# Performance work log

Hardware: AMD Instinct MI355X
Metric: run time of the kernel (lower is better)

Reference implementation:

```python
import jax, jax.numpy as jnp
import numpy as np

N = 50000
E = 600000
IN_C = 128
HID = 128
OUT_C = 2


def setup_inputs() -> dict:
    key = jax.random.key(0)
    ks = jax.random.split(key, 16)
    x = jax.random.normal(ks[0], (N, IN_C), dtype=jnp.float32)
    edge_index = jax.random.randint(ks[1], (2, E), 0, N, dtype=jnp.int64)
    s = 0.05
    # policy_net: Linear(2*in, 64) -> ReLU -> Linear(64, 1) -> Sigmoid
    W_p1 = jax.random.normal(ks[2], (64, 2 * IN_C), dtype=jnp.float32) * s
    b_p1 = jnp.zeros((64,), dtype=jnp.float32)
    W_p2 = jax.random.normal(ks[3], (1, 64), dtype=jnp.float32) * s
    b_p2 = jnp.zeros((1,), dtype=jnp.float32)
    # GCNConv weights (lin without bias + separate bias, PyG convention)
    W1 = jax.random.normal(ks[4], (HID, IN_C), dtype=jnp.float32) * s
    b1 = jnp.zeros((HID,), dtype=jnp.float32)
    W2 = jax.random.normal(ks[5], (HID, HID), dtype=jnp.float32) * s
    b2 = jnp.zeros((HID,), dtype=jnp.float32)
    W_lin = jax.random.normal(ks[6], (OUT_C, HID), dtype=jnp.float32) * s
    b_lin = jnp.zeros((OUT_C,), dtype=jnp.float32)
    return {"x": x, "edge_index": edge_index, "W_p1": W_p1, "b_p1": b_p1,
            "W_p2": W_p2, "b_p2": b_p2, "W1": W1, "b1": b1, "W2": W2,
            "b2": b2, "W_lin": W_lin, "b_lin": b_lin}


def gcn_conv(x, src, dst, edge_weight, W, b, n_nodes):
    # PyG GCNConv with normalize=True, add_self_loops=True, given edge_weight.
    loop = jnp.arange(n_nodes, dtype=src.dtype)
    s = jnp.concatenate([src, loop])
    d = jnp.concatenate([dst, loop])
    w = jnp.concatenate([edge_weight, jnp.ones((n_nodes,), x.dtype)])
    deg = jax.ops.segment_sum(w, d, num_segments=n_nodes)
    dinv = jnp.where(deg > 0, jax.lax.rsqrt(jnp.where(deg > 0, deg, 1.0)), 0.0)
    norm = dinv[s] * w * dinv[d]  # [E+N]
    xl = x @ W.T  # [N, out]
    msg = norm[:, None] * xl[s]  # gather + scale
    agg = jax.ops.segment_sum(msg, d, num_segments=n_nodes)
    return agg + b


def reference(x, edge_index, W_p1, b_p1, W_p2, b_p2, W1, b1, W2, b2, W_lin, b_lin):
    src, dst = edge_index[0], edge_index[1]
    # edge-weight policy MLP on gathered, concatenated endpoint features
    cat_feat = jnp.concatenate([x[src], x[dst]], axis=1)  # [E, 2*in]
    h = jax.nn.relu(cat_feat @ W_p1.T + b_p1)
    edge_weight = jax.nn.sigmoid(h @ W_p2.T + b_p2)[:, 0]  # [E]
    x1 = jax.nn.relu(gcn_conv(x, src, dst, edge_weight, W1, b1, N))
    x2 = jax.nn.relu(gcn_conv(x1, src, dst, edge_weight, W2, b2, N))
    out = x2 @ W_lin.T + b_lin
    return jax.nn.sigmoid(out)
```

## Files before the change

kernel.cpp:

```cpp
#include <hip/hip_runtime.h>
#include <hip/hip_bf16.h>

#define NN 50000
#define NE 600000
#define CPAD 16

typedef __attribute__((ext_vector_type(8))) short short8;
typedef __attribute__((ext_vector_type(8))) _Float16 half8;
typedef __attribute__((ext_vector_type(4))) float floatx4;

__device__ __forceinline__ short bf16_bits(float v) {
    __hip_bfloat16 h = __float2bfloat16(v);
    return *reinterpret_cast<short*>(&h);
}

__global__ void k_init_cvt(const int* __restrict__ raw, int* __restrict__ count,
                           int* __restrict__ flag, const float* __restrict__ wp1,
                           const float* __restrict__ w1, const float* __restrict__ w2,
                           __hip_bfloat16* __restrict__ wcatb, __hip_bfloat16* __restrict__ w1b,
                           __hip_bfloat16* __restrict__ w2b) {
    int i = blockIdx.x * blockDim.x + threadIdx.x;
    if (i < NN) {
        count[(size_t)i * CPAD] = 0;
    }
    if (i < 16384) {
        int r = i >> 7, c = i & 127;
        float v = (r < 64) ? wp1[r * 256 + c] : wp1[(r - 64) * 256 + 128 + c];
        wcatb[i] = __float2bfloat16(v);
    } else if (i < 32768) {
        w1b[i - 16384] = __float2bfloat16(w1[i - 16384]);
    } else if (i < 49152) {
        w2b[i - 32768] = __float2bfloat16(w2[i - 32768]);
    }
    if (blockIdx.x == 0) {
        if (threadIdx.x == 0) *flag = 0;
        __syncthreads();
        int any = 0;
        for (int j = threadIdx.x; j < 1024; j += 256) any |= raw[2 * j + 1];
        if (any) atomicOr(flag, 1);
    }
}

#define GG 782
__global__ __launch_bounds__(256) void k_uv(
    const float* __restrict__ x, const __hip_bfloat16* __restrict__ Wb,
    const float* __restrict__ bp1, _Float16* __restrict__ uvh,
    __hip_bfloat16* __restrict__ xb) {
    const int lane = threadIdx.x & 63;
    const int wave = threadIdx.x >> 6;
    const int col = lane & 15;
    const int quad = lane >> 4;

    short8 bfrag[4][8];
    const short* wp = (const short*)Wb;
#pragma unroll
    for (int tt = 0; tt < 8; ++tt) {
        int row = tt * 16 + col;
#pragma unroll
        for (int kk = 0; kk < 4; ++kk)
            bfrag[kk][tt] = *(const short8*)(wp + row * 128 + kk * 32 + quad * 8);
    }
    int tile = blockIdx.x * 4 + wave;
    if (tile >= NN / 16) return;
    int base = tile * 16;

    floatx4 acc[8];
#pragma unroll
    for (int t = 0; t < 8; ++t) acc[t] = (floatx4){0.f, 0.f, 0.f, 0.f};
#pragma unroll
    for (int kk = 0; kk < 4; ++kk) {
        const float* xrow = x + (size_t)(base + col) * 128 + kk * 32 + quad * 8;
        float4 f0 = ((const float4*)xrow)[0];
        float4 f1 = ((const float4*)xrow)[1];
        short8 afrag;
        afrag[0] = bf16_bits(f0.x); afrag[1] = bf16_bits(f0.y);
        afrag[2] = bf16_bits(f0.z); afrag[3] = bf16_bits(f0.w);
        afrag[4] = bf16_bits(f1.x); afrag[5] = bf16_bits(f1.y);
        afrag[6] = bf16_bits(f1.z); afrag[7] = bf16_bits(f1.w);
        *(short8*)((short*)xb + (size_t)(base + col) * 128 + kk * 32 + quad * 8) = afrag;
#pragma unroll
        for (int tt = 0; tt < 8; ++tt)
            acc[tt] = __builtin_amdgcn_mfma_f32_16x16x32_bf16(afrag, bfrag[kk][tt], acc[tt], 0, 0, 0);
    }
#pragma unroll
    for (int tt = 0; tt < 8; ++tt) {
        int n = tt * 16 + col;
        float badd = (tt >= 4) ? bp1[n - 64] : 0.f;
#pragma unroll
        for (int r = 0; r < 4; ++r) {
            int row = base + quad * 4 + r;
            uvh[(size_t)row * 128 + n] = (_Float16)(acc[tt][r] + badd);
        }
    }
}

#define GCNT 256
#define GPOL 9375
__global__ __launch_bounds__(256) void k_cnt_policy(
    const int* __restrict__ raw, const int* __restrict__ flag,
    int* __restrict__ count, int* __restrict__ rank,
    const _Float16* __restrict__ uvh, const float* __restrict__ wp2,
    const float* __restrict__ bp2, float* __restrict__ ew_flat) {
    const bool f32 = (*flag) != 0;
    const long long* r64 = (const long long*)raw;
    if (blockIdx.x < GCNT) {
        int tid = blockIdx.x * 256 + threadIdx.x;
        for (int e = tid; e < NE; e += GCNT * 256) {
            int d = f32 ? raw[NE + e] : (int)r64[NE + e];
            rank[e] = atomicAdd(&count[(size_t)d * CPAD], 1);
        }
        return;
    }
    int pb = blockIdx.x - GCNT;
    int wave = threadIdx.x >> 6, lane = threadIdx.x & 63;
    int g = lane >> 3, c = lane & 7;
    int e1 = pb * 64 + wave * 16 + g;
    int e2 = e1 + 8;
    int s1, d1, s2, d2;
    if (f32) {
        s1 = raw[e1]; d1 = raw[NE + e1];
        s2 = raw[e2]; d2 = raw[NE + e2];
    } else {
        s1 = (int)r64[e1]; d1 = (int)r64[NE + e1];
        s2 = (int)r64[e2]; d2 = (int)r64[NE + e2];
    }
    half8 u1 = *(const half8*)(uvh + (size_t)s1 * 128 + c * 8);
    half8 v1 = *(const half8*)(uvh + (size_t)d1 * 128 + 64 + c * 8);
    half8 u2 = *(const half8*)(uvh + (size_t)s2 * 128 + c * 8);
    half8 v2 = *(const half8*)(uvh + (size_t)d2 * 128 + 64 + c * 8);
    float w2v[8];
    const float4* w2p = (const float4*)(wp2 + c * 8);
    float4 wa = w2p[0], wb = w2p[1];
    w2v[0] = wa.x; w2v[1] = wa.y; w2v[2] = wa.z; w2v[3] = wa.w;
    w2v[4] = wb.x; w2v[5] = wb.y; w2v[6] = wb.z; w2v[7] = wb.w;
    float b2 = bp2[0];
    float p1 = 0.f, p2 = 0.f;
#pragma unroll
    for (int j = 0; j < 8; ++j) {
        float h1 = (float)u1[j] + (float)v1[j];
        float h2 = (float)u2[j] + (float)v2[j];
        h1 = h1 > 0.f ? h1 : 0.f;
        h2 = h2 > 0.f ? h2 : 0.f;
        p1 += h1 * w2v[j];
        p2 += h2 * w2v[j];
    }
    p1 += __shfl_xor(p1, 1, 64); p2 += __shfl_xor(p2, 1, 64);
    p1 += __shfl_xor(p1, 2, 64); p2 += __shfl_xor(p2, 2, 64);
    p1 += __shfl_xor(p1, 4, 64); p2 += __shfl_xor(p2, 4, 64);
    if (c == 0) {
        ew_flat[e1] = 1.f / (1.f + __expf(-(p1 + b2)));
        ew_flat[e2] = 1.f / (1.f + __expf(-(p2 + b2)));
    }
}

__global__ void k_scan_block(const int* __restrict__ count, int* __restrict__ tmp,
                             int* __restrict__ bsums) {
    __shared__ int s[512];
    int tid = threadIdx.x;
    int i = blockIdx.x * 512 + tid;
    s[tid] = (i < NN) ? count[(size_t)i * CPAD] : 0;
    __syncthreads();
    for (int off = 1; off < 512; off <<= 1) {
        int t = (tid >= off) ? s[tid - off] : 0;
        __syncthreads();
        s[tid] += t;
        __syncthreads();
    }
    if (i < NN) tmp[i] = s[tid];
    if (tid == 511) bsums[blockIdx.x] = s[511];
}

__global__ void k_finalize(const int* __restrict__ tmp, const int* __restrict__ bsums,
                           int* __restrict__ rowptr) {
    __shared__ int sb[128];
    int tid = threadIdx.x;
    if (tid < 128) sb[tid] = (tid < 98) ? bsums[tid] : 0;
    __syncthreads();
    for (int off = 1; off < 128; off <<= 1) {
        int t = (tid < 128 && tid >= off) ? sb[tid - off] : 0;
        __syncthreads();
        if (tid < 128) sb[tid] += t;
        __syncthreads();
    }
    int i = blockIdx.x * blockDim.x + tid;
    if (i >= NN) return;
    int blk = i >> 9;
    int add = blk ? sb[blk - 1] : 0;
    int incl = tmp[i] + add;
    rowptr[i + 1] = incl;
    if (i == 0) rowptr[0] = 0;
}

__global__ void k_fill(const int* __restrict__ raw, const int* __restrict__ flag,
                       const int* __restrict__ rank, const int* __restrict__ rowptr,
                       const float* __restrict__ ew_flat, int2* __restrict__ meta) {
    int e = blockIdx.x * blockDim.x + threadIdx.x;
    if (e >= NE) return;
    int s, d;
    if (*flag) {
        s = raw[e];
        d = raw[NE + e];
    } else {
        const long long* r64 = (const long long*)raw;
        s = (int)r64[e];
        d = (int)r64[NE + e];
    }
    int pos = rowptr[d] + rank[e];
    meta[pos] = make_int2(s, __float_as_int(ew_flat[e]));
}

__global__ __launch_bounds__(256) void k_deg(const int* __restrict__ rowptr,
                                             const int2* __restrict__ meta,
                                             float* __restrict__ deg) {
    int wid = (blockIdx.x * blockDim.x + threadIdx.x) >> 6;
    int lane = threadIdx.x & 63;
    if (wid >= NN) return;
    int beg = rowptr[wid], end = rowptr[wid + 1];
    float s = 0.f;
    for (int p = beg + lane; p < end; p += 64) s += __int_as_float(meta[p].y);
#pragma unroll
    for (int off = 1; off < 64; off <<= 1) s += __shfl_xor(s, off, 64);
    if (lane == 0) deg[wid] = 1.f + s;
}

__global__ __launch_bounds__(256) void k_gemm(
    const __hip_bfloat16* __restrict__ A, const __hip_bfloat16* __restrict__ Wb,
    const float* __restrict__ deg, _Float16* __restrict__ xlh) {
    const int lane = threadIdx.x & 63;
    const int wave = threadIdx.x >> 6;
    const int col = lane & 15;
    const int quad = lane >> 4;

    short8 bfrag[4][8];
    const short* wp = (const short*)Wb;
#pragma unroll
    for (int tt = 0; tt < 8; ++tt) {
        int row = tt * 16 + col;
#pragma unroll
        for (int kk = 0; kk < 4; ++kk)
            bfrag[kk][tt] = *(const short8*)(wp + row * 128 + kk * 32 + quad * 8);
    }
    int tile = blockIdx.x * 4 + wave;
    if (tile >= NN / 16) return;
    int base = tile * 16;
    const short* xs = (const short*)A;

    floatx4 acc[8];
#pragma unroll
    for (int t = 0; t < 8; ++t) acc[t] = (floatx4){0.f, 0.f, 0.f, 0.f};
#pragma unroll
    for (int kk = 0; kk < 4; ++kk) {
        short8 afrag = *(const short8*)(xs + (size_t)(base + col) * 128 + kk * 32 + quad * 8);
#pragma unroll
        for (int tt = 0; tt < 8; ++tt)
            acc[tt] = __builtin_amdgcn_mfma_f32_16x16x32_bf16(afrag, bfrag[kk][tt], acc[tt], 0, 0, 0);
    }
    float di[4];
#pragma unroll
    for (int r = 0; r < 4; ++r) di[r] = rsqrtf(deg[base + quad * 4 + r]);
#pragma unroll
    for (int tt = 0; tt < 8; ++tt) {
        int n = tt * 16 + col;
#pragma unroll
        for (int r = 0; r < 4; ++r) {
            int row = base + quad * 4 + r;
            xlh[(size_t)row * 128 + n] = (_Float16)(di[r] * acc[tt][r]);
        }
    }
}

__device__ __forceinline__ void scatter_core(
    const int* __restrict__ rowptr, const int2* __restrict__ meta,
    const _Float16* __restrict__ xlh, int wid, int g, int c, float acc[8]) {
    int beg = rowptr[wid], end = rowptr[wid + 1];
    int p = beg + g;
    for (; p + 12 < end; p += 16) {
        int2 m1 = meta[p], m2 = meta[p + 4], m3 = meta[p + 8], m4 = meta[p + 12];
        half8 r1 = *(const half8*)(xlh + (size_t)m1.x * 128 + c * 8);
        half8 r2 = *(const half8*)(xlh + (size_t)m2.x * 128 + c * 8);
        half8 r3 = *(const half8*)(xlh + (size_t)m3.x * 128 + c * 8);
        half8 r4 = *(const half8*)(xlh + (size_t)m4.x * 128 + c * 8);
        float c1 = __int_as_float(m1.y), c2 = __int_as_float(m2.y);
        float c3 = __int_as_float(m3.y), c4 = __int_as_float(m4.y);
#pragma unroll
        for (int j = 0; j < 8; ++j)
            acc[j] += c1 * (float)r1[j] + c2 * (float)r2[j] + c3 * (float)r3[j] + c4 * (float)r4[j];
    }
    for (; p + 4 < end; p += 8) {
        int2 m1 = meta[p], m2 = meta[p + 4];
        half8 r1 = *(const half8*)(xlh + (size_t)m1.x * 128 + c * 8);
        half8 r2 = *(const half8*)(xlh + (size_t)m2.x * 128 + c * 8);
        float c1 = __int_as_float(m1.y), c2 = __int_as_float(m2.y);
#pragma unroll
        for (int j = 0; j < 8; ++j) acc[j] += c1 * (float)r1[j] + c2 * (float)r2[j];
    }
    if (p < end) {
        int2 m1 = meta[p];
        half8 r1 = *(const half8*)(xlh + (size_t)m1.x * 128 + c * 8);
        float c1 = __int_as_float(m1.y);
#pragma unroll
        for (int j = 0; j < 8; ++j) acc[j] += c1 * (float)r1[j];
    }
#pragma unroll
    for (int j = 0; j < 8; ++j) {
        acc[j] += __shfl_xor(acc[j], 16, 64);
        acc[j] += __shfl_xor(acc[j], 32, 64);
    }
}

__global__ __launch_bounds__(256) void k_scatter_mid(
    const int* __restrict__ rowptr, const int2* __restrict__ meta,
    const float* __restrict__ deg, const _Float16* __restrict__ xlh,
    const float* __restrict__ bias, __hip_bfloat16* __restrict__ xb2) {
    int wid = (blockIdx.x * blockDim.x + threadIdx.x) >> 6;
    int lane = threadIdx.x & 63;
    if (wid >= NN) return;
    int g = lane >> 4, c = lane & 15;
    float acc[8] = {0.f, 0.f, 0.f, 0.f, 0.f, 0.f, 0.f, 0.f};
    scatter_core(rowptr, meta, xlh, wid, g, c, acc);
    if (g == 0) {
        float dn = rsqrtf(deg[wid]);
        half8 sv = *(const half8*)(xlh + (size_t)wid * 128 + c * 8);
        const float4* bp = (const float4*)(bias + c * 8);
        float4 ba = bp[0], bb = bp[1];
        float bv[8] = {ba.x, ba.y, ba.z, ba.w, bb.x, bb.y, bb.z, bb.w};
        short8 o;
#pragma unroll
        for (int j = 0; j < 8; ++j) {
            float t = bv[j] + dn * ((float)sv[j] + acc[j]);
            t = t > 0.f ? t : 0.f;
            o[j] = bf16_bits(t);
        }
        *(short8*)((short*)xb2 + (size_t)wid * 128 + c * 8) = o;
    }
}

__global__ __launch_bounds__(256) void k_scatter_out(
    const int* __restrict__ rowptr, const int2* __restrict__ meta,
    const float* __restrict__ deg, const _Float16* __restrict__ xlh,
    const float* __restrict__ bias, const float* __restrict__ wlin,
    const float* __restrict__ blin, float* __restrict__ out) {
    int wid = (blockIdx.x * blockDim.x + threadIdx.x) >> 6;
    int lane = threadIdx.x & 63;
    if (wid >= NN) return;
    int g = lane >> 4, c = lane & 15;
    float acc[8] = {0.f, 0.f, 0.f, 0.f, 0.f, 0.f, 0.f, 0.f};
    scatter_core(rowptr, meta, xlh, wid, g, c, acc);
    if (g == 0) {
        float dn = rsqrtf(deg[wid]);
        half8 sv = *(const half8*)(xlh + (size_t)wid * 128 + c * 8);
        const float4* bp = (const float4*)(bias + c * 8);
        float4 ba = bp[0], bb = bp[1];
        float bv[8] = {ba.x, ba.y, ba.z, ba.w, bb.x, bb.y, bb.z, bb.w};
        float p0 = 0.f, p1 = 0.f;
#pragma unroll
        for (int j = 0; j < 8; ++j) {
            float t = bv[j] + dn * ((float)sv[j] + acc[j]);
            t = t > 0.f ? t : 0.f;
            p0 += t * wlin[c * 8 + j];
            p1 += t * wlin[128 + c * 8 + j];
        }
#pragma unroll
        for (int off = 1; off < 16; off <<= 1) {
            p0 += __shfl_xor(p0, off, 64);
            p1 += __shfl_xor(p1, off, 64);
        }
        if (c == 0) {
            out[wid * 2 + 0] = 1.f / (1.f + __expf(-(p0 + blin[0])));
            out[wid * 2 + 1] = 1.f / (1.f + __expf(-(p1 + blin[1])));
        }
    }
}


extern "C" void kernel_launch(void* const* d_in, const int* in_sizes, int n_in,
                              void* d_out, int out_size, void* d_ws, size_t ws_size,
                              hipStream_t stream) {
    const float* x = (const float*)d_in[0];
    const int* eidx_raw = (const int*)d_in[1];
    const float* W_p1 = (const float*)d_in[2];
    const float* b_p1 = (const float*)d_in[3];
    const float* W_p2 = (const float*)d_in[4];
    const float* b_p2 = (const float*)d_in[5];
    const float* W1 = (const float*)d_in[6];
    const float* b1 = (const float*)d_in[7];
    const float* W2 = (const float*)d_in[8];
    const float* b2 = (const float*)d_in[9];
    const float* W_lin = (const float*)d_in[10];
    const float* b_lin = (const float*)d_in[11];
    float* out = (float*)d_out;

    char* ws = (char*)d_ws;
    size_t off = 0;
    auto alloc = [&](size_t bytes) -> void* {
        off = (off + 255) & ~(size_t)255;
        void* p = ws + off;
        off += bytes;
        return p;
    };
    float* deg = (float*)alloc(NN * 4);
    int* rowptr = (int*)alloc((NN + 1) * 4);
    int* count = (int*)alloc((size_t)NN * CPAD * 4);
    int* flag = (int*)alloc(4);
    int* bsums = (int*)alloc(128 * 4);
    int* rank = (int*)alloc((size_t)NE * 4);
    float* ew_flat = (float*)alloc((size_t)NE * 4);
    int2* meta = (int2*)alloc((size_t)NE * 8);
    __hip_bfloat16* xb = (__hip_bfloat16*)alloc((size_t)NN * 128 * 2);
    _Float16* xlh = (_Float16*)alloc((size_t)NN * 128 * 2);
    _Float16* uvh = (_Float16*)alloc((size_t)NN * 128 * 2);
    __hip_bfloat16* wcatb = (__hip_bfloat16*)alloc(128 * 128 * 2);
    __hip_bfloat16* w1b = (__hip_bfloat16*)alloc(128 * 128 * 2);
    __hip_bfloat16* w2b = (__hip_bfloat16*)alloc(128 * 128 * 2);
    int* tmp = (int*)meta;

    const int TB = 256;
    int gN = (NN + TB - 1) / TB;
    int gE = (NE + TB - 1) / TB;
    int gS = (NN + 3) / 4;

    k_init_cvt<<<gN, TB, 0, stream>>>(eidx_raw, count, flag, W_p1, W1, W2, wcatb, w1b, w2b);
    k_uv<<<GG, TB, 0, stream>>>(x, wcatb, b_p1, uvh, xb);
    k_cnt_policy<<<GCNT + GPOL, TB, 0, stream>>>(eidx_raw, flag, count, rank, uvh, W_p2, b_p2, ew_flat);

    k_scan_block<<<98, 512, 0, stream>>>(count, tmp, bsums);
    k_finalize<<<gN, TB, 0, stream>>>(tmp, bsums, rowptr);
    k_fill<<<gE, TB, 0, stream>>>(eidx_raw, flag, rank, rowptr, ew_flat, meta);
    k_deg<<<gS, TB, 0, stream>>>(rowptr, meta, deg);

    k_gemm<<<GG, TB, 0, stream>>>(xb, w1b, deg, xlh);
    k_scatter_mid<<<gS, TB, 0, stream>>>(rowptr, meta, deg, xlh, b1, xb);
    k_gemm<<<GG, TB, 0, stream>>>(xb, w2b, deg, xlh);
    k_scatter_out<<<gS, TB, 0, stream>>>(rowptr, meta, deg, xlh, b2, W_lin, b_lin, out);
}
```

Before: 277.5 us.

## Fuse init, scan, and degree kernels to cut launch count

Removes the separate init/convert kernel by converting fp32 weights to bf16 inside each GEMM wave and doing the count zeroing and flag detection in extra blocks of k_uv. The two scan kernels merge into one single-pass scan that uses decoupled look-back on bsums. Degree computation moves into the first GEMM. The counting path now handles 8 edges per thread. This drops four launches and some intermediate traffic, but every wave redundantly converts weights. The look-back spin-wait relies on all 98 blocks being co-resident and on bsums being zeroed in an earlier kernel.

```diff
diff --git a/kernel.cpp b/kernel.cpp
--- a/kernel.cpp
+++ b/kernel.cpp
@@ -14,69 +14,65 @@
     return *reinterpret_cast<short*>(&h);
 }
 
-__global__ void k_init_cvt(const int* __restrict__ raw, int* __restrict__ count,
-                           int* __restrict__ flag, const float* __restrict__ wp1,
-                           const float* __restrict__ w1, const float* __restrict__ w2,
-                           __hip_bfloat16* __restrict__ wcatb, __hip_bfloat16* __restrict__ w1b,
-                           __hip_bfloat16* __restrict__ w2b) {
-    int i = blockIdx.x * blockDim.x + threadIdx.x;
-    if (i < NN) {
-        count[(size_t)i * CPAD] = 0;
-    }
-    if (i < 16384) {
-        int r = i >> 7, c = i & 127;
-        float v = (r < 64) ? wp1[r * 256 + c] : wp1[(r - 64) * 256 + 128 + c];
-        wcatb[i] = __float2bfloat16(v);
-    } else if (i < 32768) {
-        w1b[i - 16384] = __float2bfloat16(w1[i - 16384]);
-    } else if (i < 49152) {
-        w2b[i - 32768] = __float2bfloat16(w2[i - 32768]);
-    }
-    if (blockIdx.x == 0) {
-        if (threadIdx.x == 0) *flag = 0;
-        __syncthreads();
-        int any = 0;
-        for (int j = threadIdx.x; j < 1024; j += 256) any |= raw[2 * j + 1];
-        if (any) atomicOr(flag, 1);
-    }
+__device__ __forceinline__ short8 cvt8(const float* src) {
+    float4 a0 = ((const float4*)src)[0];
+    float4 a1 = ((const float4*)src)[1];
+    short8 f;
+    f[0] = bf16_bits(a0.x); f[1] = bf16_bits(a0.y);
+    f[2] = bf16_bits(a0.z); f[3] = bf16_bits(a0.w);
+    f[4] = bf16_bits(a1.x); f[5] = bf16_bits(a1.y);
+    f[6] = bf16_bits(a1.z); f[7] = bf16_bits(a1.w);
+    return f;
 }
 
 #define GG 782
+#define GAUX 196
 __global__ __launch_bounds__(256) void k_uv(
-    const float* __restrict__ x, const __hip_bfloat16* __restrict__ Wb,
+    const float* __restrict__ x, const float* __restrict__ wp1,
     const float* __restrict__ bp1, _Float16* __restrict__ uvh,
-    __hip_bfloat16* __restrict__ xb) {
+    __hip_bfloat16* __restrict__ xb, const int* __restrict__ raw,
+    int* __restrict__ count, int* __restrict__ bsums, int* __restrict__ flag) {
+    if (blockIdx.x >= GG) {
+        int a = blockIdx.x - GG;
+        int i = a * 256 + threadIdx.x;
+        if (i < NN) count[(size_t)i * CPAD] = 0;
+        if (a == 0) {
+            if (threadIdx.x < 98) bsums[threadIdx.x] = 0;
+            if (threadIdx.x == 0) *flag = 0;
+            __syncthreads();
+            int any = 0;
+            for (int j = threadIdx.x; j < 1024; j += 256) any |= raw[2 * j + 1];
+            if (any) atomicOr(flag, 1);
+        }
+        return;
+    }
     const int lane = threadIdx.x & 63;
     const int wave = threadIdx.x >> 6;
     const int col = lane & 15;
     const int quad = lane >> 4;
 
-    short8 bfrag[4][8];
-    const short* wp = (const short*)Wb;
-#pragma unroll
-    for (int tt = 0; tt < 8; ++tt) {
-        int row = tt * 16 + col;
-#pragma unroll
-        for (int kk = 0; kk < 4; ++kk)
-            bfrag[kk][tt] = *(const short8*)(wp + row * 128 + kk * 32 + quad * 8);
-    }
     int tile = blockIdx.x * 4 + wave;
     if (tile >= NN / 16) return;
     int base = tile * 16;
 
+    short8 bfrag[4][8];
+#pragma unroll
+    for (int tt = 0; tt < 8; ++tt) {
+        int row = tt * 16 + col;
+        const float* src = (tt < 4) ? (wp1 + (size_t)row * 256)
+                                    : (wp1 + (size_t)(row - 64) * 256 + 128);
+#pragma unroll
+        for (int kk = 0; kk < 4; ++kk)
+            bfrag[kk][tt] = cvt8(src + kk * 32 + quad * 8);
+    }
+
     floatx4 acc[8];
 #pragma unroll
     for (int t = 0; t < 8; ++t) acc[t] = (floatx4){0.f, 0.f, 0.f, 0.f};
 #pragma unroll
     for (int kk = 0; kk < 4; ++kk) {
         const float* xrow = x + (size_t)(base + col) * 128 + kk * 32 + quad * 8;
-        float4 f0 = ((const float4*)xrow)[0];
-        float4 f1 = ((const float4*)xrow)[1];
-        short8 afrag;
-        afrag[0] = bf16_bits(f0.x); afrag[1] = bf16_bits(f0.y);
-        afrag[2] = bf16_bits(f0.z); afrag[3] = bf16_bits(f0.w);
-        afrag[4] = bf16_bits(f1.x); afrag[5] = bf16_bits(f1.y);
-        afrag[6] = bf16_bits(f1.z); afrag[7] = bf16_bits(f1.w);
+        short8 afrag = cvt8(xrow);
         *(short8*)((short*)xb + (size_t)(base + col) * 128 + kk * 32 + quad * 8) = afrag;
 #pragma unroll
         for (int tt = 0; tt < 8; ++tt)
@@ -94,7 +90,7 @@
     }
 }
 
-#define GCNT 256
+#define GCNT 293
 #define GPOL 9375
 __global__ __launch_bounds__(256) void k_cnt_policy(
     const int* __restrict__ raw, const int* __restrict__ flag,
@@ -104,10 +100,27 @@
     const bool f32 = (*flag) != 0;
     const long long* r64 = (const long long*)raw;
     if (blockIdx.x < GCNT) {
-        int tid = blockIdx.x * 256 + threadIdx.x;
-        for (int e = tid; e < NE; e += GCNT * 256) {
-            int d = f32 ? raw[NE + e] : (int)r64[NE + e];
-            rank[e] = atomicAdd(&count[(size_t)d * CPAD], 1);
+        int gid = blockIdx.x * 256 + threadIdx.x;
+        int e0 = gid * 8;
+        if (e0 + 8 <= NE) {
+            int dd[8];
+            if (f32) {
+#pragma unroll
+                for (int k = 0; k < 8; ++k) dd[k] = raw[NE + e0 + k];
+            } else {
+#pragma unroll
+                for (int k = 0; k < 8; ++k) dd[k] = (int)r64[NE + e0 + k];
+            }
+            int rk[8];
+#pragma unroll
+            for (int k = 0; k < 8; ++k) rk[k] = atomicAdd(&count[(size_t)dd[k] * CPAD], 1);
+#pragma unroll
+            for (int k = 0; k < 8; ++k) rank[e0 + k] = rk[k];
+        } else {
+            for (int e = e0; e < NE; ++e) {
+                int d = f32 ? raw[NE + e] : (int)r64[NE + e];
+                rank[e] = atomicAdd(&count[(size_t)d * CPAD], 1);
+            }
         }
         return;
     }
@@ -153,11 +166,12 @@
     }
 }
 
-__global__ void k_scan_block(const int* __restrict__ count, int* __restrict__ tmp,
-                             int* __restrict__ bsums) {
+__global__ __launch_bounds__(512) void k_scan_rowptr(
+    const int* __restrict__ count, int* __restrict__ bsums, int* __restrict__ rowptr) {
     __shared__ int s[512];
-    int tid = threadIdx.x;
-    int i = blockIdx.x * 512 + tid;
+    __shared__ int red[512];
+    int tid = threadIdx.x, bid = blockIdx.x;
+    int i = bid * 512 + tid;
     s[tid] = (i < NN) ? count[(size_t)i * CPAD] : 0;
     __syncthreads();
     for (int off = 1; off < 512; off <<= 1) {
@@ -166,29 +180,22 @@
         s[tid] += t;
         __syncthreads();
     }
-    if (i < NN) tmp[i] = s[tid];
-    if (tid == 511) bsums[blockIdx.x] = s[511];
-}
-
-__global__ void k_finalize(const int* __restrict__ tmp, const int* __restrict__ bsums,
-                           int* __restrict__ rowptr) {
-    __shared__ int sb[128];
-    int tid = threadIdx.x;
-    if (tid < 128) sb[tid] = (tid < 98) ? bsums[tid] : 0;
+    if (tid == 511) atomicExch(&bsums[bid], s[511] + 1);
+    int part = 0;
+    for (int j = tid; j < bid; j += 512) {
+        int v;
+        do { v = atomicAdd(&bsums[j], 0); } while (v == 0);
+        part += v - 1;
+    }
+    red[tid] = part;
     __syncthreads();
-    for (int off = 1; off < 128; off <<= 1) {
-        int t = (tid < 128 && tid >= off) ? sb[tid - off] : 0;
+    for (int off = 256; off > 0; off >>= 1) {
+        if (tid < off) red[tid] += red[tid + off];
         __syncthreads();
-        if (tid < 128) sb[tid] += t;
-        __syncthreads();
-    }
-    int i = blockIdx.x * blockDim.x + tid;
-    if (i >= NN) return;
-    int blk = i >> 9;
-    int add = blk ? sb[blk - 1] : 0;
-    int incl = tmp[i] + add;
-    rowptr[i + 1] = incl;
-    if (i == 0) rowptr[0] = 0;
+    }
+    int prefix = red[0];
+    if (i < NN) rowptr[i + 1] = s[tid] + prefix;
+    if (bid == 0 && tid == 0) rowptr[0] = 0;
 }
 
 __global__ void k_fill(const int* __restrict__ raw, const int* __restrict__ flag,
@@ -209,40 +216,28 @@
     meta[pos] = make_int2(s, __float_as_int(ew_flat[e]));
 }
 
-__global__ __launch_bounds__(256) void k_deg(const int* __restrict__ rowptr,
-                                             const int2* __restrict__ meta,
-                                             float* __restrict__ deg) {
-    int wid = (blockIdx.x * blockDim.x + threadIdx.x) >> 6;
-    int lane = threadIdx.x & 63;
-    if (wid >= NN) return;
-    int beg = rowptr[wid], end = rowptr[wid + 1];
-    float s = 0.f;
-    for (int p = beg + lane; p < end; p += 64) s += __int_as_float(meta[p].y);
-#pragma unroll
-    for (int off = 1; off < 64; off <<= 1) s += __shfl_xor(s, off, 64);
-    if (lane == 0) deg[wid] = 1.f + s;
-}
-
+template <bool CDEG>
 __global__ __launch_bounds__(256) void k_gemm(
-    const __hip_bfloat16* __restrict__ A, const __hip_bfloat16* __restrict__ Wb,
-    const float* __restrict__ deg, _Float16* __restrict__ xlh) {
+    const __hip_bfloat16* __restrict__ A, const float* __restrict__ W,
+    const int* __restrict__ rowptr, const int2* __restrict__ meta,
+    float* __restrict__ deg, _Float16* __restrict__ xlh) {
     const int lane = threadIdx.x & 63;
     const int wave = threadIdx.x >> 6;
     const int col = lane & 15;
     const int quad = lane >> 4;
 
-    short8 bfrag[4][8];
-    const short* wp = (const short*)Wb;
-#pragma unroll
-    for (int tt = 0; tt < 8; ++tt) {
-        int row = tt * 16 + col;
-#pragma unroll
-        for (int kk = 0; kk < 4; ++kk)
-            bfrag[kk][tt] = *(const short8*)(wp + row * 128 + kk * 32 + quad * 8);
-    }
     int tile = blockIdx.x * 4 + wave;
     if (tile >= NN / 16) return;
     int base = tile * 16;
+
+    short8 bfrag[4][8];
+#pragma unroll
+    for (int tt = 0; tt < 8; ++tt) {
+        int row = tt * 16 + col;
+#pragma unroll
+        for (int kk = 0; kk < 4; ++kk)
+            bfrag[kk][tt] = cvt8(W + (size_t)row * 128 + kk * 32 + quad * 8);
+    }
     const short* xs = (const short*)A;
 
     floatx4 acc[8];
@@ -256,8 +251,21 @@
             acc[tt] = __builtin_amdgcn_mfma_f32_16x16x32_bf16(afrag, bfrag[kk][tt], acc[tt], 0, 0, 0);
     }
     float di[4];
-#pragma unroll
-    for (int r = 0; r < 4; ++r) di[r] = rsqrtf(deg[base + quad * 4 + r]);
+    if (CDEG) {
+        int rn = base + col;
+        int beg = rowptr[rn], end = rowptr[rn + 1];
+        float sdeg = 0.f;
+        for (int p = beg + quad; p < end; p += 4) sdeg += __int_as_float(meta[p].y);
+        sdeg += __shfl_xor(sdeg, 16, 64);
+        sdeg += __shfl_xor(sdeg, 32, 64);
+        float dv = 1.f + sdeg;
+        if (quad == 0) deg[rn] = dv;
+#pragma unroll
+        for (int r = 0; r < 4; ++r) di[r] = rsqrtf(__shfl(dv, quad * 4 + r, 64));
+    } else {
+#pragma unroll
+        for (int r = 0; r < 4; ++r) di[r] = rsqrtf(deg[base + quad * 4 + r]);
+    }
 #pragma unroll
     for (int tt = 0; tt < 8; ++tt) {
         int n = tt * 16 + col;
@@ -409,27 +417,17 @@
     __hip_bfloat16* xb = (__hip_bfloat16*)alloc((size_t)NN * 128 * 2);
     _Float16* xlh = (_Float16*)alloc((size_t)NN * 128 * 2);
     _Float16* uvh = (_Float16*)alloc((size_t)NN * 128 * 2);
-    __hip_bfloat16* wcatb = (__hip_bfloat16*)alloc(128 * 128 * 2);
-    __hip_bfloat16* w1b = (__hip_bfloat16*)alloc(128 * 128 * 2);
-    __hip_bfloat16* w2b = (__hip_bfloat16*)alloc(128 * 128 * 2);
-    int* tmp = (int*)meta;
 
     const int TB = 256;
-    int gN = (NN + TB - 1) / TB;
     int gE = (NE + TB - 1) / TB;
     int gS = (NN + 3) / 4;
 
-    k_init_cvt<<<gN, TB, 0, stream>>>(eidx_raw, count, flag, W_p1, W1, W2, wcatb, w1b, w2b);
-    k_uv<<<GG, TB, 0, stream>>>(x, wcatb, b_p1, uvh, xb);
+    k_uv<<<GG + GAUX, TB, 0, stream>>>(x, W_p1, b_p1, uvh, xb, eidx_raw, count, bsums, flag);
     k_cnt_policy<<<GCNT + GPOL, TB, 0, stream>>>(eidx_raw, flag, count, rank, uvh, W_p2, b_p2, ew_flat);
-
-    k_scan_block<<<98, 512, 0, stream>>>(count, tmp, bsums);
-    k_finalize<<<gN, TB, 0, stream>>>(tmp, bsums, rowptr);
+    k_scan_rowptr<<<98, 512, 0, stream>>>(count, bsums, rowptr);
     k_fill<<<gE, TB, 0, stream>>>(eidx_raw, flag, rank, rowptr, ew_flat, meta);
-    k_deg<<<gS, TB, 0, stream>>>(rowptr, meta, deg);
-
-    k_gemm<<<GG, TB, 0, stream>>>(xb, w1b, deg, xlh);
+    k_gemm<true><<<GG, TB, 0, stream>>>(xb, W1, rowptr, meta, deg, xlh);
     k_scatter_mid<<<gS, TB, 0, stream>>>(rowptr, meta, deg, xlh, b1, xb);
-    k_gemm<<<GG, TB, 0, stream>>>(xb, w2b, deg, xlh);
+    k_gemm<false><<<GG, TB, 0, stream>>>(xb, W2, rowptr, meta, deg, xlh);
     k_scatter_out<<<gS, TB, 0, stream>>>(rowptr, meta, deg, xlh, b2, W_lin, b_lin, out);
 }
```

New measurement: 311.0 us. 1.12x slower.

## Stage weights in swizzled LDS for GEMMs and batch edge-count atomics per thread

Applied to the files above, without the earlier changes.

The two MFMA GEMM kernels now load the 128x128 bf16 weight matrix into LDS once per block with cooperative coalesced loads and an XOR swizzle. Each wave then reads its B fragments from LDS instead of issuing scattered 16-byte global loads per lane. The edge-count part of the counting kernel now handles 8 consecutive edges per thread, issuing all loads and then all atomics back to back to raise memory-level parallelism. The changes add 32KB of LDS per block and a block-wide barrier, which can lower occupancy, and the block count for the counting section changes to cover the edges.

```diff
diff --git a/kernel.cpp b/kernel.cpp
--- a/kernel.cpp
+++ b/kernel.cpp
@@ -12,6 +12,17 @@
 __device__ __forceinline__ short bf16_bits(float v) {
     __hip_bfloat16 h = __float2bfloat16(v);
     return *reinterpret_cast<short*>(&h);
+}
+
+__device__ __forceinline__ void stage_w(const short* __restrict__ src, short* lds) {
+    int t = threadIdx.x;
+#pragma unroll
+    for (int i = 0; i < 8; ++i) {
+        int gci = t + i * 256;
+        int row = gci >> 4, ci = gci & 15;
+        short8 v = *(const short8*)(src + gci * 8);
+        *(short8*)(lds + row * 128 + ((ci ^ (row & 7)) << 3)) = v;
+    }
 }
 
 __global__ void k_init_cvt(const int* __restrict__ raw, int* __restrict__ count,
@@ -46,23 +57,28 @@
     const float* __restrict__ x, const __hip_bfloat16* __restrict__ Wb,
     const float* __restrict__ bp1, _Float16* __restrict__ uvh,
     __hip_bfloat16* __restrict__ xb) {
+    __shared__ short wlds[16384];
+    stage_w((const short*)Wb, wlds);
+    __syncthreads();
+
     const int lane = threadIdx.x & 63;
     const int wave = threadIdx.x >> 6;
     const int col = lane & 15;
     const int quad = lane >> 4;
 
-    short8 bfrag[4][8];
-    const short* wp = (const short*)Wb;
-#pragma unroll
-    for (int tt = 0; tt < 8; ++tt) {
-        int row = tt * 16 + col;
-#pragma unroll
-        for (int kk = 0; kk < 4; ++kk)
-            bfrag[kk][tt] = *(const short8*)(wp + row * 128 + kk * 32 + quad * 8);
-    }
     int tile = blockIdx.x * 4 + wave;
     if (tile >= NN / 16) return;
     int base = tile * 16;
+
+    short8 bfrag[4][8];
+    const int rx = col & 7;
+#pragma unroll
+    for (int tt = 0; tt < 8; ++tt) {
+        int row = tt * 16 + col;
+#pragma unroll
+        for (int kk = 0; kk < 4; ++kk)
+            bfrag[kk][tt] = *(const short8*)(wlds + row * 128 + (((kk * 4 + quad) ^ rx) << 3));
+    }
 
     floatx4 acc[8];
 #pragma unroll
@@ -94,7 +110,7 @@
     }
 }
 
-#define GCNT 256
+#define GCNT 293
 #define GPOL 9375
 __global__ __launch_bounds__(256) void k_cnt_policy(
     const int* __restrict__ raw, const int* __restrict__ flag,
@@ -104,10 +120,27 @@
     const bool f32 = (*flag) != 0;
     const long long* r64 = (const long long*)raw;
     if (blockIdx.x < GCNT) {
-        int tid = blockIdx.x * 256 + threadIdx.x;
-        for (int e = tid; e < NE; e += GCNT * 256) {
-            int d = f32 ? raw[NE + e] : (int)r64[NE + e];
-            rank[e] = atomicAdd(&count[(size_t)d * CPAD], 1);
+        int gid = blockIdx.x * 256 + threadIdx.x;
+        int e0 = gid * 8;
+        if (e0 + 8 <= NE) {
+            int dd[8];
+            if (f32) {
+#pragma unroll
+                for (int k = 0; k < 8; ++k) dd[k] = raw[NE + e0 + k];
+            } else {
+#pragma unroll
+                for (int k = 0; k < 8; ++k) dd[k] = (int)r64[NE + e0 + k];
+            }
+            int rk[8];
+#pragma unroll
+            for (int k = 0; k < 8; ++k) rk[k] = atomicAdd(&count[(size_t)dd[k] * CPAD], 1);
+#pragma unroll
+            for (int k = 0; k < 8; ++k) rank[e0 + k] = rk[k];
+        } else {
+            for (int e = e0; e < NE; ++e) {
+                int d = f32 ? raw[NE + e] : (int)r64[NE + e];
+                rank[e] = atomicAdd(&count[(size_t)d * CPAD], 1);
+            }
         }
         return;
     }
@@ -226,23 +259,28 @@
 __global__ __launch_bounds__(256) void k_gemm(
     const __hip_bfloat16* __restrict__ A, const __hip_bfloat16* __restrict__ Wb,
     const float* __restrict__ deg, _Float16* __restrict__ xlh) {
+    __shared__ short wlds[16384];
+    stage_w((const short*)Wb, wlds);
+    __syncthreads();
+
     const int lane = threadIdx.x & 63;
     const int wave = threadIdx.x >> 6;
     const int col = lane & 15;
     const int quad = lane >> 4;
 
-    short8 bfrag[4][8];
-    const short* wp = (const short*)Wb;
-#pragma unroll
-    for (int tt = 0; tt < 8; ++tt) {
-        int row = tt * 16 + col;
-#pragma unroll
-        for (int kk = 0; kk < 4; ++kk)
-            bfrag[kk][tt] = *(const short8*)(wp + row * 128 + kk * 32 + quad * 8);
-    }
     int tile = blockIdx.x * 4 + wave;
     if (tile >= NN / 16) return;
     int base = tile * 16;
+
+    short8 bfrag[4][8];
+    const int rx = col & 7;
+#pragma unroll
+    for (int tt = 0; tt < 8; ++tt) {
+        int row = tt * 16 + col;
+#pragma unroll
+        for (int kk = 0; kk < 4; ++kk)
+            bfrag[kk][tt] = *(const short8*)(wlds + row * 128 + (((kk * 4 + quad) ^ rx) << 3));
+    }
     const short* xs = (const short*)A;
 
     floatx4 acc[8];
```

Result: faster. 244.0 us (-12.1%).
